# Optimization experiments

Hardware: AMD Instinct MI355X
Metric: run time of the kernel (lower is better)

## Reference

```python
import jax, jax.numpy as jnp
import numpy as np

N_HEAD = 8
N_EMBD = 768
T_MAX = 1024


def setup_inputs() -> dict:
    key = jax.random.key(0)
    ks = jax.random.split(key, 5)
    B, T, C = 8, 1024, N_EMBD
    x = jax.random.normal(ks[0], (B, T, C), dtype=jnp.float32)
    c_attn_weight = jax.random.normal(ks[1], (3 * C, C), dtype=jnp.float32) * (1.0 / np.sqrt(C))
    c_attn_bias = jax.random.normal(ks[2], (3 * C,), dtype=jnp.float32) * 0.02
    c_proj_weight = jax.random.normal(ks[3], (C, C), dtype=jnp.float32) * (1.0 / np.sqrt(C))
    c_proj_bias = jax.random.normal(ks[4], (C,), dtype=jnp.float32) * 0.02
    bias = jnp.tril(jnp.ones((T_MAX, T_MAX), dtype=jnp.int32))[None, None]  # (1,1,Tmax,Tmax)
    return {
        "x": x,
        "c_attn_weight": c_attn_weight,
        "c_attn_bias": c_attn_bias,
        "c_proj_weight": c_proj_weight,
        "c_proj_bias": c_proj_bias,
        "bias": bias,
    }


def reference(x, c_attn_weight, c_attn_bias, c_proj_weight, c_proj_bias, bias):
    B, T, C = x.shape
    H = N_HEAD
    D = C // H  # head dim
    qkv = jnp.einsum("btc,fc->btf", x, c_attn_weight) + c_attn_bias  # (B,T,3C)
    q, k, v = jnp.split(qkv, 3, axis=-1)
    q = q.reshape(B, T, H, D).transpose(0, 2, 1, 3)  # (B,H,T,D)
    k = k.reshape(B, T, H, D).transpose(0, 2, 1, 3)
    v = v.reshape(B, T, H, D).transpose(0, 2, 1, 3)
    att = jnp.einsum("bhqd,bhkd->bhqk", q, k) * (1.0 / np.sqrt(D))  # (B,H,T,T)
    mask = bias[:, :, :T, :T] == 0
    att = jnp.where(mask, jnp.float32(-jnp.inf), att)
    att = jax.nn.softmax(att, axis=-1)
    y = jnp.einsum("bhqk,bhkd->bhqd", att, v)  # (B,H,T,D)
    y = y.transpose(0, 2, 1, 3).reshape(B, T, C)
    y = jnp.einsum("btc,fc->btf", y, c_proj_weight) + c_proj_bias
    return y
```

## Files before the change

kernel.cpp:

```cpp
#include <hip/hip_runtime.h>
#include <hip/hip_bf16.h>
#include <stdint.h>


typedef unsigned short ushort_t;
typedef __attribute__((ext_vector_type(8))) short short8;
typedef __attribute__((ext_vector_type(4))) float floatx4;
typedef __attribute__((ext_vector_type(4))) unsigned short ushort4v;

#define MFMA16(a, b, c) __builtin_amdgcn_mfma_f32_16x16x32_bf16(a, b, c, 0, 0, 0)
#define NEG_BIG (-1e30f)

__device__ __forceinline__ unsigned short f2bf(float f) {
  union { float f; unsigned int u; } v; v.f = f;
  unsigned int r = (v.u + 0x7FFFu + ((v.u >> 16) & 1u)) >> 16;
  return (unsigned short)r;
}

__device__ __forceinline__ unsigned int packbf2(float a, float b) {
  union { __hip_bfloat162 h; unsigned int u; } cv;
  cv.h = __float22bfloat162_rn(make_float2(a, b));
  return cv.u;
}

#define GLOAD16(src, dst)                                              \
  __builtin_amdgcn_global_load_lds(                                    \
      (const __attribute__((address_space(1))) void*)(src),            \
      (__attribute__((address_space(3))) void*)(dst), 16, 0, 0)

__global__ __launch_bounds__(256) void cvt3(
    const float* __restrict__ x, const float* __restrict__ wa,
    const float* __restrict__ wp, ushort_t* __restrict__ xb,
    ushort_t* __restrict__ wab, ushort_t* __restrict__ wpb)
{
  const int n1 = (8192 * 768) / 4, n2 = (2304 * 768) / 4;
  int i = blockIdx.x * 256 + threadIdx.x;
  const float* in; ushort_t* out;
  if (i < n1)            { in = x;  out = xb; }
  else if (i < n1 + n2)  { in = wa; out = wab; i -= n1; }
  else                   { in = wp; out = wpb; i -= (n1 + n2); }
  float4 v = *(const float4*)(in + (size_t)i * 4);
  ushort4v o;
  o.x = f2bf(v.x); o.y = f2bf(v.y); o.z = f2bf(v.z); o.w = f2bf(v.w);
  *(ushort4v*)(out + (size_t)i * 4) = o;
}

__global__ __launch_bounds__(256) void gemm_qkv(
    const ushort_t* __restrict__ A,
    const ushort_t* __restrict__ W,
    const float* __restrict__ bias,
    ushort_t* __restrict__ QK,
    ushort_t* __restrict__ VT)
{
  const int K = 768;
  __shared__ ushort_t As[2][128 * 32];
  __shared__ ushort_t Bs[2][128 * 32];

  const int tid  = threadIdx.x;
  const int lane = tid & 63;
  const int l15  = lane & 15;
  const int quad = lane >> 4;
  const int wid  = tid >> 6;
  const int m0 = blockIdx.x * 128;
  const int n0 = blockIdx.y * 128;
  const int wm = (wid >> 1) * 64;
  const int wn = (wid & 1) * 64;
  const int srow = tid >> 2;
  const int scol = (tid & 3) * 8;

  floatx4 acc[4][4] = {};

  const ushort_t* gA = A + (size_t)(m0 + srow) * K + scol;
  const ushort_t* gB = W + (size_t)(n0 + srow) * K + scol;

  {
    ushort_t* lA = &As[0][wid * 512];
    ushort_t* lB = &Bs[0][wid * 512];
    GLOAD16(gA, lA);
    GLOAD16(gA + (size_t)64 * K, lA + 64 * 32);
    GLOAD16(gB, lB);
    GLOAD16(gB + (size_t)64 * K, lB + 64 * 32);
  }
  __syncthreads();

  int cur = 0;
  for (int k0 = 0; k0 < K; k0 += 32) {
    if (k0 + 32 < K) {
      ushort_t* lA = &As[cur ^ 1][wid * 512];
      ushort_t* lB = &Bs[cur ^ 1][wid * 512];
      const ushort_t* pA = gA + k0 + 32;
      const ushort_t* pB = gB + k0 + 32;
      GLOAD16(pA, lA);
      GLOAD16(pA + (size_t)64 * K, lA + 64 * 32);
      GLOAD16(pB, lB);
      GLOAD16(pB + (size_t)64 * K, lB + 64 * 32);
    }

    short8 af[4], bf[4];
#pragma unroll
    for (int t = 0; t < 4; ++t)
      af[t] = *(const short8*)&As[cur][(wm + t * 16 + l15) * 32 + quad * 8];
#pragma unroll
    for (int t = 0; t < 4; ++t)
      bf[t] = *(const short8*)&Bs[cur][(wn + t * 16 + l15) * 32 + quad * 8];
#pragma unroll
    for (int tm = 0; tm < 4; ++tm)
#pragma unroll
      for (int tn = 0; tn < 4; ++tn)
        acc[tm][tn] = MFMA16(af[tm], bf[tn], acc[tm][tn]);
    __syncthreads();
    cur ^= 1;
  }

  const float QSCALE = 0.10206207261596577f * 1.4426950408889634f;

#pragma unroll
  for (int tn = 0; tn < 4; ++tn) {
    const int gc = n0 + wn + tn * 16 + l15;
    const float bv = bias[gc];
    const bool isv = (gc >= 1536);
    const bool isq = (gc < 768);
    const int hh = (gc - 1536) / 96, dd = (gc - 1536) % 96;
#pragma unroll
    for (int tm = 0; tm < 4; ++tm) {
      const int gr = m0 + wm + tm * 16 + quad * 4;
#pragma unroll
      for (int r = 0; r < 4; ++r) {
        float val = acc[tm][tn][r] + bv;
        const int row = gr + r;
        if (!isv) {
          if (isq) val *= QSCALE;
          QK[(size_t)row * 1536 + gc] = f2bf(val);
        } else {
          const int bb = row >> 10, tt = row & 1023;
          const int tt2 = (tt & ~0x1C) | (((tt >> 4) & 1) << 2) |
                          (((tt >> 2) & 3) << 3);
          VT[(((size_t)(bb * 8 + hh)) * 96 + dd) * 1024 + tt2] = f2bf(val);
        }
      }
    }
  }
}

__global__ __launch_bounds__(256) void gemm_proj(
    const ushort_t* __restrict__ A,
    const ushort_t* __restrict__ W,
    const float* __restrict__ bias,
    float* __restrict__ C,
    int M, int N, int K)
{
  __shared__ ushort_t As[2][128 * 32];
  __shared__ ushort_t Bs[2][128 * 32];

  const int tid  = threadIdx.x;
  const int lane = tid & 63;
  const int l15  = lane & 15;
  const int quad = lane >> 4;
  const int wid  = tid >> 6;
  const int m0 = blockIdx.x * 128;
  const int n0 = blockIdx.y * 128;
  const int wm = (wid >> 1) * 64;
  const int wn = (wid & 1) * 64;
  const int srow = tid >> 2;
  const int scol = (tid & 3) * 8;

  floatx4 acc[4][4] = {};

  const ushort_t* gA = A + (size_t)(m0 + srow) * K + scol;
  const ushort_t* gB = W + (size_t)(n0 + srow) * K + scol;

  {
    ushort_t* lA = &As[0][wid * 512];
    ushort_t* lB = &Bs[0][wid * 512];
    GLOAD16(gA, lA);
    GLOAD16(gA + (size_t)64 * K, lA + 64 * 32);
    GLOAD16(gB, lB);
    GLOAD16(gB + (size_t)64 * K, lB + 64 * 32);
  }
  __syncthreads();

  int cur = 0;
  for (int k0 = 0; k0 < K; k0 += 32) {
    if (k0 + 32 < K) {
      ushort_t* lA = &As[cur ^ 1][wid * 512];
      ushort_t* lB = &Bs[cur ^ 1][wid * 512];
      const ushort_t* pA = gA + k0 + 32;
      const ushort_t* pB = gB + k0 + 32;
      GLOAD16(pA, lA);
      GLOAD16(pA + (size_t)64 * K, lA + 64 * 32);
      GLOAD16(pB, lB);
      GLOAD16(pB + (size_t)64 * K, lB + 64 * 32);
    }

    short8 af[4], bf[4];
#pragma unroll
    for (int t = 0; t < 4; ++t)
      af[t] = *(const short8*)&As[cur][(wm + t * 16 + l15) * 32 + quad * 8];
#pragma unroll
    for (int t = 0; t < 4; ++t)
      bf[t] = *(const short8*)&Bs[cur][(wn + t * 16 + l15) * 32 + quad * 8];
#pragma unroll
    for (int tm = 0; tm < 4; ++tm)
#pragma unroll
      for (int tn = 0; tn < 4; ++tn)
        acc[tm][tn] = MFMA16(af[tm], bf[tn], acc[tm][tn]);
    __syncthreads();
    cur ^= 1;
  }

#pragma unroll
  for (int tn = 0; tn < 4; ++tn) {
    const int gc = n0 + wn + tn * 16 + l15;
    const float bv = bias[gc];
#pragma unroll
    for (int tm = 0; tm < 4; ++tm) {
      const int gr = m0 + wm + tm * 16 + quad * 4;
#pragma unroll
      for (int r = 0; r < 4; ++r)
        C[(size_t)(gr + r) * N + gc] = acc[tm][tn][r] + bv;
    }
  }
}

__global__ __launch_bounds__(256) void attn_fused(
    const ushort_t* __restrict__ QK,
    const ushort_t* __restrict__ VT,
    ushort_t* __restrict__ y)
{
  __shared__ ushort_t Ks[2][64 * 96];
  __shared__ ushort_t Vt[2][96 * 72];

  const int tid  = threadIdx.x;
  const int lane = tid & 63;
  const int l15  = lane & 15;
  const int quad = lane >> 4;
  const int wid  = tid >> 6;
  const int bh = blockIdx.y;
  const int b = bh >> 3;
  const int h = bh & 7;
  const int qoff = h * 96;

  const int cA = blockIdx.x;
  const int cB = 31 - cA;
  const int myChunk = (wid < 2) ? cA : cB;
  const int q0w = myChunk * 32 + (wid & 1) * 16;
  const int kend = cB * 32 + 32;
  const int rq = q0w + l15;

  const size_t rowbase = (size_t)b * 1024;
  const ushort_t* vtb = VT + (size_t)bh * 96 * 1024;

  const int ke0 = wid * 1536 + lane * 8;
  const int vd  = (tid >> 3);
  const int vkc = (tid & 7) * 8;

  short8 qf[3];
#pragma unroll
  for (int c = 0; c < 3; ++c)
    qf[c] = *(const short8*)(QK + (rowbase + q0w + l15) * 1536 + qoff +
                             c * 32 + quad * 8);

  float m_i = NEG_BIG;
  float l_i = 0.f;
  floatx4 O[6] = {};

  {
#pragma unroll
    for (int i = 0; i < 3; ++i) {
      const int e = ke0 + i * 512;
      const int kr = e / 96, kc = e % 96;
      GLOAD16(QK + (rowbase + kr) * 1536 + 768 + qoff + kc,
              &Ks[0][wid * 1536 + i * 512]);
    }
#pragma unroll
    for (int g = 0; g < 3; ++g) {
      const int d = g * 32 + vd;
      short8 v = *(const short8*)(vtb + (size_t)d * 1024 + vkc);
      *(short8*)&Vt[0][d * 72 + vkc] = v;
    }
  }
  __syncthreads();

  int cur = 0;
  for (int k0 = 0; k0 < kend; k0 += 64) {
    const int nk = k0 + 64;
    const bool more = (nk < kend);

    short8 vreg[3];
    if (more) {
#pragma unroll
      for (int i = 0; i < 3; ++i) {
        const int e = ke0 + i * 512;
        const int kr = e / 96, kc = e % 96;
        GLOAD16(QK + (rowbase + nk + kr) * 1536 + 768 + qoff + kc,
                &Ks[cur ^ 1][wid * 1536 + i * 512]);
      }
#pragma unroll
      for (int g = 0; g < 3; ++g)
        vreg[g] = *(const short8*)(vtb + (size_t)(g * 32 + vd) * 1024 + nk + vkc);
    }

    if (k0 < q0w + 16) {
      floatx4 s[4] = {};
#pragma unroll
      for (int t = 0; t < 4; ++t) {
#pragma unroll
        for (int c = 0; c < 3; ++c) {
          short8 kf = *(const short8*)
              &Ks[cur][(t * 16 + l15) * 96 + c * 32 + quad * 8];
          s[t] = MFMA16(kf, qf[c], s[t]);
        }
      }
      float p[4][4];
      if (k0 + 64 <= q0w) {
#pragma unroll
        for (int t = 0; t < 4; ++t)
#pragma unroll
          for (int j = 0; j < 4; ++j) p[t][j] = s[t][j];
      } else {
        const int kq = k0 + quad * 4;
#pragma unroll
        for (int t = 0; t < 4; ++t)
#pragma unroll
          for (int j = 0; j < 4; ++j)
            p[t][j] = (kq + t * 16 + j <= rq) ? s[t][j] : NEG_BIG;
      }
      float m0v = fmaxf(fmaxf(p[0][0], p[0][1]), fmaxf(p[0][2], p[0][3]));
      float m1v = fmaxf(fmaxf(p[1][0], p[1][1]), fmaxf(p[1][2], p[1][3]));
      float m2v = fmaxf(fmaxf(p[2][0], p[2][1]), fmaxf(p[2][2], p[2][3]));
      float m3v = fmaxf(fmaxf(p[3][0], p[3][1]), fmaxf(p[3][2], p[3][3]));
      float mt = fmaxf(fmaxf(m0v, m1v), fmaxf(m2v, m3v));
      mt = fmaxf(mt, __shfl_xor(mt, 16));
      mt = fmaxf(mt, __shfl_xor(mt, 32));
      if (!__all(mt - m_i <= 8.0f)) {
        const float mn = fmaxf(m_i, mt);
        const float al = __builtin_amdgcn_exp2f(m_i - mn);
        m_i = mn;
        l_i *= al;
#pragma unroll
        for (int j = 0; j < 4; ++j) {
          const float alr = __shfl(al, quad * 4 + j);
#pragma unroll
          for (int f = 0; f < 6; ++f) O[f][j] *= alr;
        }
      }
      float rs = 0.f;
#pragma unroll
      for (int t = 0; t < 4; ++t)
#pragma unroll
        for (int j = 0; j < 4; ++j) {
          p[t][j] = __builtin_amdgcn_exp2f(p[t][j] - m_i);
          rs += p[t][j];
        }
      rs += __shfl_xor(rs, 16);
      rs += __shfl_xor(rs, 32);
      l_i += rs;
      union { short8 s8; unsigned int u[4]; } pf0, pf1;
      pf0.u[0] = packbf2(p[0][0], p[0][1]);
      pf0.u[1] = packbf2(p[0][2], p[0][3]);
      pf0.u[2] = packbf2(p[1][0], p[1][1]);
      pf0.u[3] = packbf2(p[1][2], p[1][3]);
      pf1.u[0] = packbf2(p[2][0], p[2][1]);
      pf1.u[1] = packbf2(p[2][2], p[2][3]);
      pf1.u[2] = packbf2(p[3][0], p[3][1]);
      pf1.u[3] = packbf2(p[3][2], p[3][3]);
#pragma unroll
      for (int f = 0; f < 6; ++f) {
        short8 vf0 = *(const short8*)&Vt[cur][(f * 16 + l15) * 72 + quad * 8];
        O[f] = MFMA16(pf0.s8, vf0, O[f]);
        short8 vf1 = *(const short8*)
            &Vt[cur][(f * 16 + l15) * 72 + 32 + quad * 8];
        O[f] = MFMA16(pf1.s8, vf1, O[f]);
      }
    }

    if (more) {
#pragma unroll
      for (int g = 0; g < 3; ++g)
        *(short8*)&Vt[cur ^ 1][(g * 32 + vd) * 72 + vkc] = vreg[g];
    }
    __syncthreads();
    cur ^= 1;
  }

  float inv[4];
#pragma unroll
  for (int j = 0; j < 4; ++j) {
    const float lj = __shfl(l_i, quad * 4 + j);
    inv[j] = 1.0f / fmaxf(lj, 1e-20f);
  }
#pragma unroll
  for (int j = 0; j < 4; ++j) {
    const size_t row = rowbase + q0w + quad * 4 + j;
#pragma unroll
    for (int f = 0; f < 6; ++f)
      y[row * 768 + qoff + f * 16 + l15] = f2bf(O[f][j] * inv[j]);
  }
}

extern "C" void kernel_launch(void* const* d_in, const int* in_sizes, int n_in,
                              void* d_out, int out_size, void* d_ws, size_t ws_size,
                              hipStream_t stream)
{
  const float* x_f  = (const float*)d_in[0];
  const float* wa_f = (const float*)d_in[1];
  const float* ba_f = (const float*)d_in[2];
  const float* wp_f = (const float*)d_in[3];
  const float* bp_f = (const float*)d_in[4];
  float* out = (float*)d_out;

  ushort_t* xb  = (ushort_t*)d_ws;
  ushort_t* wab = xb  + (size_t)8192 * 768;
  ushort_t* wpb = wab + (size_t)2304 * 768;
  ushort_t* QK  = wpb + (size_t)768 * 768;
  ushort_t* VT  = QK  + (size_t)8192 * 1536;
  ushort_t* yw  = VT  + (size_t)8192 * 768;

  cvt3<<<8448, 256, 0, stream>>>(x_f, wa_f, wp_f, xb, wab, wpb);

  gemm_qkv<<<dim3(64, 18), 256, 0, stream>>>(xb, wab, ba_f, QK, VT);
  attn_fused<<<dim3(16, 64), 256, 0, stream>>>(QK, VT, yw);
  gemm_proj<<<dim3(64, 6), 256, 0, stream>>>(yw, wpb, bp_f, out,
                                             8192, 768, 768);
}
```

Before: 227.6 us.

## Triple-buffer GEMM LDS pipelines with swizzle and deepen attention V prefetch

Both GEMMs move from double to triple buffering of the A/B LDS tiles. They prefetch two K-steps ahead and synchronise with explicit s_waitcnt vmcnt plus s_barrier instead of __syncthreads. An XOR swizzle is applied to the LDS tile columns, on both the global-to-LDS load side and the fragment read side, to reduce bank conflicts. In the attention kernel, V tiles are prefetched into registers one tile further ahead, and the loop barrier moves to the top with explicit vmcnt and lgkmcnt waits, so global latency overlaps more with compute. The costs are more LDS per GEMM block, which may lower occupancy, and hand-counted waitcnt values that must match the exact load order.

```diff
diff --git a/kernel.cpp b/kernel.cpp
--- a/kernel.cpp
+++ b/kernel.cpp
@@ -27,6 +27,22 @@
   __builtin_amdgcn_global_load_lds(                                    \
       (const __attribute__((address_space(1))) void*)(src),            \
       (__attribute__((address_space(3))) void*)(dst), 16, 0, 0)
+
+#define WAITBAR(VM)                                                    \
+  do {                                                                 \
+    asm volatile("s_waitcnt vmcnt(" #VM ")" ::: "memory");             \
+    __builtin_amdgcn_sched_barrier(0);                                 \
+    __builtin_amdgcn_s_barrier();                                      \
+    __builtin_amdgcn_sched_barrier(0);                                 \
+  } while (0)
+
+#define WAITBAR_LGKM(VM)                                               \
+  do {                                                                 \
+    asm volatile("s_waitcnt vmcnt(" #VM ") lgkmcnt(0)" ::: "memory");  \
+    __builtin_amdgcn_sched_barrier(0);                                 \
+    __builtin_amdgcn_s_barrier();                                      \
+    __builtin_amdgcn_sched_barrier(0);                                 \
+  } while (0)
 
 __global__ __launch_bounds__(256) void cvt3(
     const float* __restrict__ x, const float* __restrict__ wa,
@@ -45,6 +61,33 @@
   *(ushort4v*)(out + (size_t)i * 4) = o;
 }
 
+#define GEMM_STAGE(BUF, OFF)                                           \
+  do {                                                                 \
+    ushort_t* lA = &As[BUF][wid * 512];                                \
+    ushort_t* lB = &Bs[BUF][wid * 512];                                \
+    const ushort_t* pA = gA + (OFF);                                   \
+    const ushort_t* pB = gB + (OFF);                                   \
+    GLOAD16(pA, lA);                                                   \
+    GLOAD16(pA + (size_t)64 * 768, lA + 64 * 32);                      \
+    GLOAD16(pB, lB);                                                   \
+    GLOAD16(pB + (size_t)64 * 768, lB + 64 * 32);                      \
+  } while (0)
+
+#define GEMM_COMPUTE(BUF)                                              \
+  do {                                                                 \
+    short8 af[4], bf[4];                                               \
+    _Pragma("unroll")                                                  \
+    for (int t_ = 0; t_ < 4; ++t_) {                                   \
+      af[t_] = *(const short8*)&As[BUF][(wm + t_ * 16 + l15) * 32 + sw]; \
+      bf[t_] = *(const short8*)&Bs[BUF][(wn + t_ * 16 + l15) * 32 + sw]; \
+    }                                                                  \
+    _Pragma("unroll")                                                  \
+    for (int tm = 0; tm < 4; ++tm)                                     \
+      _Pragma("unroll")                                                \
+      for (int tn = 0; tn < 4; ++tn)                                   \
+        acc[tm][tn] = MFMA16(af[tm], bf[tn], acc[tm][tn]);             \
+  } while (0)
+
 __global__ __launch_bounds__(256) void gemm_qkv(
     const ushort_t* __restrict__ A,
     const ushort_t* __restrict__ W,
@@ -53,8 +96,8 @@
     ushort_t* __restrict__ VT)
 {
   const int K = 768;
-  __shared__ ushort_t As[2][128 * 32];
-  __shared__ ushort_t Bs[2][128 * 32];
+  __shared__ ushort_t As[3][128 * 32];
+  __shared__ ushort_t Bs[3][128 * 32];
 
   const int tid  = threadIdx.x;
   const int lane = tid & 63;
@@ -66,50 +109,26 @@
   const int wm = (wid >> 1) * 64;
   const int wn = (wid & 1) * 64;
   const int srow = tid >> 2;
-  const int scol = (tid & 3) * 8;
+  const int scol = (((tid & 3) ^ ((srow ^ (srow >> 2)) & 3))) * 8;
+  const int sw = (quad ^ ((l15 ^ (l15 >> 2)) & 3)) * 8;
 
   floatx4 acc[4][4] = {};
 
   const ushort_t* gA = A + (size_t)(m0 + srow) * K + scol;
   const ushort_t* gB = W + (size_t)(n0 + srow) * K + scol;
 
-  {
-    ushort_t* lA = &As[0][wid * 512];
-    ushort_t* lB = &Bs[0][wid * 512];
-    GLOAD16(gA, lA);
-    GLOAD16(gA + (size_t)64 * K, lA + 64 * 32);
-    GLOAD16(gB, lB);
-    GLOAD16(gB + (size_t)64 * K, lB + 64 * 32);
-  }
-  __syncthreads();
-
-  int cur = 0;
-  for (int k0 = 0; k0 < K; k0 += 32) {
-    if (k0 + 32 < K) {
-      ushort_t* lA = &As[cur ^ 1][wid * 512];
-      ushort_t* lB = &Bs[cur ^ 1][wid * 512];
-      const ushort_t* pA = gA + k0 + 32;
-      const ushort_t* pB = gB + k0 + 32;
-      GLOAD16(pA, lA);
-      GLOAD16(pA + (size_t)64 * K, lA + 64 * 32);
-      GLOAD16(pB, lB);
-      GLOAD16(pB + (size_t)64 * K, lB + 64 * 32);
-    }
-
-    short8 af[4], bf[4];
-#pragma unroll
-    for (int t = 0; t < 4; ++t)
-      af[t] = *(const short8*)&As[cur][(wm + t * 16 + l15) * 32 + quad * 8];
-#pragma unroll
-    for (int t = 0; t < 4; ++t)
-      bf[t] = *(const short8*)&Bs[cur][(wn + t * 16 + l15) * 32 + quad * 8];
-#pragma unroll
-    for (int tm = 0; tm < 4; ++tm)
-#pragma unroll
-      for (int tn = 0; tn < 4; ++tn)
-        acc[tm][tn] = MFMA16(af[tm], bf[tn], acc[tm][tn]);
-    __syncthreads();
-    cur ^= 1;
+  GEMM_STAGE(0, 0);
+  GEMM_STAGE(1, 32);
+
+  int bc = 0;
+  for (int t = 0; t < 24; ++t) {
+    if (t < 23) WAITBAR(4); else WAITBAR(0);
+    if (t + 2 < 24) {
+      const int bs = (bc >= 1) ? bc - 1 : 2;
+      GEMM_STAGE(bs, (t + 2) * 32);
+    }
+    GEMM_COMPUTE(bc);
+    bc = (bc < 2) ? bc + 1 : 0;
   }
 
   const float QSCALE = 0.10206207261596577f * 1.4426950408889634f;
@@ -147,10 +166,11 @@
     const ushort_t* __restrict__ W,
     const float* __restrict__ bias,
     float* __restrict__ C,
-    int M, int N, int K)
+    int M, int N)
 {
-  __shared__ ushort_t As[2][128 * 32];
-  __shared__ ushort_t Bs[2][128 * 32];
+  const int K = 768;
+  __shared__ ushort_t As[3][128 * 32];
+  __shared__ ushort_t Bs[3][128 * 32];
 
   const int tid  = threadIdx.x;
   const int lane = tid & 63;
@@ -162,50 +182,26 @@
   const int wm = (wid >> 1) * 64;
   const int wn = (wid & 1) * 64;
   const int srow = tid >> 2;
-  const int scol = (tid & 3) * 8;
+  const int scol = (((tid & 3) ^ ((srow ^ (srow >> 2)) & 3))) * 8;
+  const int sw = (quad ^ ((l15 ^ (l15 >> 2)) & 3)) * 8;
 
   floatx4 acc[4][4] = {};
 
   const ushort_t* gA = A + (size_t)(m0 + srow) * K + scol;
   const ushort_t* gB = W + (size_t)(n0 + srow) * K + scol;
 
-  {
-    ushort_t* lA = &As[0][wid * 512];
-    ushort_t* lB = &Bs[0][wid * 512];
-    GLOAD16(gA, lA);
-    GLOAD16(gA + (size_t)64 * K, lA + 64 * 32);
-    GLOAD16(gB, lB);
-    GLOAD16(gB + (size_t)64 * K, lB + 64 * 32);
-  }
-  __syncthreads();
-
-  int cur = 0;
-  for (int k0 = 0; k0 < K; k0 += 32) {
-    if (k0 + 32 < K) {
-      ushort_t* lA = &As[cur ^ 1][wid * 512];
-      ushort_t* lB = &Bs[cur ^ 1][wid * 512];
-      const ushort_t* pA = gA + k0 + 32;
-      const ushort_t* pB = gB + k0 + 32;
-      GLOAD16(pA, lA);
-      GLOAD16(pA + (size_t)64 * K, lA + 64 * 32);
-      GLOAD16(pB, lB);
-      GLOAD16(pB + (size_t)64 * K, lB + 64 * 32);
-    }
-
-    short8 af[4], bf[4];
-#pragma unroll
-    for (int t = 0; t < 4; ++t)
-      af[t] = *(const short8*)&As[cur][(wm + t * 16 + l15) * 32 + quad * 8];
-#pragma unroll
-    for (int t = 0; t < 4; ++t)
-      bf[t] = *(const short8*)&Bs[cur][(wn + t * 16 + l15) * 32 + quad * 8];
-#pragma unroll
-    for (int tm = 0; tm < 4; ++tm)
-#pragma unroll
-      for (int tn = 0; tn < 4; ++tn)
-        acc[tm][tn] = MFMA16(af[tm], bf[tn], acc[tm][tn]);
-    __syncthreads();
-    cur ^= 1;
+  GEMM_STAGE(0, 0);
+  GEMM_STAGE(1, 32);
+
+  int bc = 0;
+  for (int t = 0; t < 24; ++t) {
+    if (t < 23) WAITBAR(4); else WAITBAR(0);
+    if (t + 2 < 24) {
+      const int bs = (bc >= 1) ? bc - 1 : 2;
+      GEMM_STAGE(bs, (t + 2) * 32);
+    }
+    GEMM_COMPUTE(bc);
+    bc = (bc < 2) ? bc + 1 : 0;
   }
 
 #pragma unroll
@@ -264,29 +260,32 @@
   float l_i = 0.f;
   floatx4 O[6] = {};
 
-  {
-#pragma unroll
-    for (int i = 0; i < 3; ++i) {
-      const int e = ke0 + i * 512;
-      const int kr = e / 96, kc = e % 96;
-      GLOAD16(QK + (rowbase + kr) * 1536 + 768 + qoff + kc,
-              &Ks[0][wid * 1536 + i * 512]);
-    }
-#pragma unroll
-    for (int g = 0; g < 3; ++g) {
-      const int d = g * 32 + vd;
-      short8 v = *(const short8*)(vtb + (size_t)d * 1024 + vkc);
-      *(short8*)&Vt[0][d * 72 + vkc] = v;
-    }
-  }
-  __syncthreads();
+  short8 vreg[3];
+
+#pragma unroll
+  for (int g = 0; g < 3; ++g)
+    vreg[g] = *(const short8*)(vtb + (size_t)(g * 32 + vd) * 1024 + vkc);
+#pragma unroll
+  for (int i = 0; i < 3; ++i) {
+    const int e = ke0 + i * 512;
+    const int kr = e / 96, kc = e % 96;
+    GLOAD16(QK + (rowbase + kr) * 1536 + 768 + qoff + kc,
+            &Ks[0][wid * 1536 + i * 512]);
+  }
+#pragma unroll
+  for (int g = 0; g < 3; ++g)
+    *(short8*)&Vt[0][(g * 32 + vd) * 72 + vkc] = vreg[g];
+#pragma unroll
+  for (int g = 0; g < 3; ++g)
+    vreg[g] = *(const short8*)(vtb + (size_t)(g * 32 + vd) * 1024 + 64 + vkc);
 
   int cur = 0;
   for (int k0 = 0; k0 < kend; k0 += 64) {
     const int nk = k0 + 64;
     const bool more = (nk < kend);
 
-    short8 vreg[3];
+    if (more) WAITBAR_LGKM(3); else WAITBAR_LGKM(0);
+
     if (more) {
 #pragma unroll
       for (int i = 0; i < 3; ++i) {
@@ -295,9 +294,6 @@
         GLOAD16(QK + (rowbase + nk + kr) * 1536 + 768 + qoff + kc,
                 &Ks[cur ^ 1][wid * 1536 + i * 512]);
       }
-#pragma unroll
-      for (int g = 0; g < 3; ++g)
-        vreg[g] = *(const short8*)(vtb + (size_t)(g * 32 + vd) * 1024 + nk + vkc);
     }
 
     if (k0 < q0w + 16) {
@@ -378,8 +374,13 @@
 #pragma unroll
       for (int g = 0; g < 3; ++g)
         *(short8*)&Vt[cur ^ 1][(g * 32 + vd) * 72 + vkc] = vreg[g];
-    }
-    __syncthreads();
+      if (nk + 64 < kend) {
+#pragma unroll
+        for (int g = 0; g < 3; ++g)
+          vreg[g] = *(const short8*)
+              (vtb + (size_t)(g * 32 + vd) * 1024 + nk + 64 + vkc);
+      }
+    }
     cur ^= 1;
   }
 
@@ -421,5 +422,5 @@
   gemm_qkv<<<dim3(64, 18), 256, 0, stream>>>(xb, wab, ba_f, QK, VT);
   attn_fused<<<dim3(16, 64), 256, 0, stream>>>(QK, VT, yw);
   gemm_proj<<<dim3(64, 6), 256, 0, stream>>>(yw, wpb, bp_f, out,
-                                             8192, 768, 768);
-}
+                                             8192, 768);
+}
```

Result: no change. 224.8 us (-1.2%).
